# Kernel tuning notes

Measured on AMD Instinct MI355X. Metric: run time of the kernel, lower is better.

## Reference

```python
import jax, jax.numpy as jnp
import numpy as np

B, L, C = 2, 2048, 1024
DK, H = 64, 16

def setup_inputs() -> dict:
    key = jax.random.key(0)
    ks = jax.random.split(key, 12)
    def lin(kw, kb, out_dim, in_dim):
        w = jax.random.normal(kw, (out_dim, in_dim), jnp.float32) * (1.0 / np.sqrt(in_dim))
        b = jnp.zeros((out_dim,), jnp.float32)
        return w, b
    WQ_w, WQ_b = lin(ks[0], ks[1], DK * H, C)
    WK_w, WK_b = lin(ks[2], ks[3], DK * H, C)
    WV_w, WV_b = lin(ks[4], ks[5], DK * H, C)
    WO_w, WO_b = lin(ks[6], ks[7], C, DK * H)
    qx = jax.random.normal(ks[8], (B, L, C), jnp.float32)
    kx = jax.random.normal(ks[9], (B, L, C), jnp.float32)
    vx = jax.random.normal(ks[10], (B, L, C), jnp.float32)
    maskPAD = jax.random.randint(ks[11], (B, L, L), 0, 2, jnp.int32)
    return {"qx": qx, "kx": kx, "vx": vx, "maskPAD": maskPAD,
            "WQ_w": WQ_w, "WQ_b": WQ_b, "WK_w": WK_w, "WK_b": WK_b,
            "WV_w": WV_w, "WV_b": WV_b, "WO_w": WO_w, "WO_b": WO_b}

def reference(qx, kx, vx, maskPAD, WQ_w, WQ_b, WK_w, WK_b, WV_w, WV_b, WO_w, WO_b):
    Bq, qL, _ = qx.shape
    kvL = kx.shape[1]
    # projections -> [B, H, L, DK]
    q = (qx @ WQ_w.T + WQ_b).reshape(Bq, qL, H, DK).transpose(0, 2, 1, 3)
    k = (kx @ WK_w.T + WK_b).reshape(Bq, kvL, H, DK).transpose(0, 2, 1, 3)
    v = (vx @ WV_w.T + WV_b).reshape(Bq, kvL, H, DK).transpose(0, 2, 1, 3)
    scores = jnp.einsum('bhqd,bhkd->bhqk', q, k) / np.sqrt(DK).astype(np.float32)
    scores = jnp.where((maskPAD == 0)[:, None, :, :], jnp.float32(-2**15 + 1), scores)
    alpha = jax.nn.softmax(scores, axis=3)  # dropout p=0 (eval)
    z = jnp.einsum('bhqk,bhkd->bhqd', alpha, v)
    z = z.transpose(0, 2, 1, 3).reshape(Bq, qL, H * DK)
    return z @ WO_w.T + WO_b
```

## Files before the change

kernel.cpp:

```cpp
#include <hip/hip_runtime.h>
#include <stdint.h>
#include <math.h>

typedef short short8 __attribute__((ext_vector_type(8)));
typedef float float4v __attribute__((ext_vector_type(4)));

static __device__ __forceinline__ float bf2f(uint16_t u) {
    union { uint32_t i; float f; } x; x.i = ((uint32_t)u) << 16; return x.f;
}
static __device__ __forceinline__ uint16_t f2bf(float f) {
    union { float f; uint32_t i; } x; x.f = f;
    uint32_t u = x.i;
    u += 0x7FFFu + ((u >> 16) & 1u);
    return (uint16_t)(u >> 16);
}
static __device__ __forceinline__ uint16_t f2bf_sane(float f) {
    uint16_t u = f2bf(f);
    if ((u & 0x7F80u) == 0x7F80u) u = 0;
    return u;
}
static __device__ __forceinline__ float san_f32(float f) {
    union { float f; uint32_t i; } x; x.f = f;
    if (((x.i >> 23) & 0xFFu) == 0xFFu) return 0.f;
    return x.f;
}
static __device__ __forceinline__ void gll16(const void* g, void* l) {
    __builtin_amdgcn_global_load_lds((const __attribute__((address_space(1))) void*)g,
                                     (__attribute__((address_space(3))) void*)l,
                                     16, 0, 0);
}
static __device__ __forceinline__ short8 load8(const void* p, size_t off, int fp32) {
    if (!fp32) return *(const short8*)((const uint16_t*)p + off);
    const float* f = (const float*)p + off;
    const float4v a = *(const float4v*)f;
    const float4v b = *(const float4v*)(f + 4);
    short8 r;
    r[0] = (short)f2bf(a[0]); r[1] = (short)f2bf(a[1]);
    r[2] = (short)f2bf(a[2]); r[3] = (short)f2bf(a[3]);
    r[4] = (short)f2bf(b[0]); r[5] = (short)f2bf(b[1]);
    r[6] = (short)f2bf(b[2]); r[7] = (short)f2bf(b[3]);
    return r;
}

__global__ __launch_bounds__(256) void detect_kernel(const uint16_t* qx, int* flag)
{
    __shared__ int s;
    const int tid = threadIdx.x;
    if (tid == 0) s = 0;
    __syncthreads();
    int bad = 0;
#pragma unroll 8
    for (int i = 0; i < 64; ++i) {
        const uint16_t u = qx[tid * 64 + i];
        bad |= ((u & 0x7F80u) == 0x7F80u) ? 1 : 0;
    }
    if (bad) atomicOr(&s, 1);
    __syncthreads();
    if (tid == 0) *flag = s;
}

__global__ __launch_bounds__(256) void pack_kernel(
    const int* __restrict__ mask, uint64_t* __restrict__ mask64)
{
    const int wave = threadIdx.x >> 6, lane = threadIdx.x & 63;
    const int row = blockIdx.x * 4 + wave;
    const int* src = mask + (size_t)row * 2048;
#pragma unroll 4
    for (int j = 0; j < 32; ++j) {
        const int m = src[j * 64 + lane];
        const uint64_t bal = __ballot(m != 0);
        if (lane == 0) mask64[(size_t)row * 32 + j] = bal;
    }
}

__global__ __launch_bounds__(256) void convert_kernel(
    const void* qx, const void* kx, const void* vx,
    const void* wq, const void* wk, const void* wv, const void* wo,
    const void* bq, const void* bk, const void* bv, const void* bo,
    uint16_t* cIn, uint16_t* cW, uint16_t* cB, const int* flag)
{
    const int mode = *flag;
    if (!mode) return;
    const int z = blockIdx.z;
    const int idx8 = blockIdx.x * 256 + threadIdx.x;
    if (z < 3) {
        const void* src = (z == 0) ? qx : (z == 1) ? kx : vx;
        uint16_t* dst = cIn + (size_t)z * 4194304;
        if (idx8 < 524288)
            *(short8*)(dst + (size_t)idx8 * 8) = load8(src, (size_t)idx8 * 8, 1);
    } else if (z < 7) {
        const int t = z - 3;
        const void* src = (t == 0) ? wq : (t == 1) ? wk : (t == 2) ? wv : wo;
        uint16_t* dst = cW + (size_t)t * 1048576;
        if (idx8 < 131072)
            *(short8*)(dst + (size_t)idx8 * 8) = load8(src, (size_t)idx8 * 8, 1);
    } else {
        if (idx8 < 128) {
#pragma unroll
            for (int t = 0; t < 4; ++t) {
                const void* src = (t == 0) ? bq : (t == 1) ? bk : (t == 2) ? bv : bo;
                *(short8*)(cB + t * 1024 + idx8 * 8) = load8(src, (size_t)idx8 * 8, 1);
            }
        }
    }
}

template <int MI, int NI>
static __device__ __forceinline__ void gemm_tile(
    const uint16_t* __restrict__ A, const uint16_t* __restrict__ W,
    const uint16_t* __restrict__ bias, void* __restrict__ C,
    int c_fp32, float out_scale)
{
    constexpr int TM = MI * 32, TN = NI * 32;
    __shared__ __align__(16) uint16_t sA[TM * 32];
    __shared__ __align__(16) uint16_t sB[TN * 32];

    const int tid  = threadIdx.x;
    const int wave = tid >> 6;
    const int lane = tid & 63;
    const int quad = lane >> 4;
    const int l15  = lane & 15;
    const int m0 = blockIdx.y * TM;
    const int n0 = blockIdx.x * TN;
    const int wm = (wave >> 1) * (MI * 16);
    const int wn = (wave & 1) * (NI * 16);
    const int r16 = lane >> 2;
    const int ch  = lane & 3;

    float4v acc[MI][NI] = {};

    for (int k0 = 0; k0 < 1024; k0 += 32) {
        __syncthreads();
#pragma unroll
        for (int g = wave; g < TM / 16; g += 4)
            gll16(A + (size_t)(m0 + g * 16 + r16) * 1024 + k0 + ch * 8,
                  (char*)sA + (size_t)g * 1024);
#pragma unroll
        for (int g = wave; g < TN / 16; g += 4)
            gll16(W + (size_t)(n0 + g * 16 + r16) * 1024 + k0 + ch * 8,
                  (char*)sB + (size_t)g * 1024);
        asm volatile("s_waitcnt vmcnt(0)" ::: "memory");
        __syncthreads();

        short8 af[MI], bfr[NI];
#pragma unroll
        for (int i = 0; i < MI; ++i)
            af[i] = *(const short8*)&sA[(wm + i * 16 + l15) * 32 + quad * 8];
#pragma unroll
        for (int j = 0; j < NI; ++j)
            bfr[j] = *(const short8*)&sB[(wn + j * 16 + l15) * 32 + quad * 8];
#pragma unroll
        for (int mi = 0; mi < MI; ++mi)
#pragma unroll
            for (int ni = 0; ni < NI; ++ni)
                acc[mi][ni] = __builtin_amdgcn_mfma_f32_16x16x32_bf16(
                    af[mi], bfr[ni], acc[mi][ni], 0, 0, 0);
    }

#pragma unroll
    for (int ni = 0; ni < NI; ++ni) {
        const int n = n0 + wn + ni * 16 + l15;
        const float bv = bf2f(bias[n]);
#pragma unroll
        for (int mi = 0; mi < MI; ++mi) {
            const int mbase = m0 + wm + mi * 16 + quad * 4;
#pragma unroll
            for (int r = 0; r < 4; ++r) {
                const float v = (acc[mi][ni][r] + bv) * out_scale;
                const size_t idx = (size_t)(mbase + r) * 1024 + n;
                if (c_fp32) ((float*)C)[idx] = san_f32(v);
                else        ((uint16_t*)C)[idx] = f2bf_sane(v);
            }
        }
    }
}

__global__ __launch_bounds__(256) void qkv_kernel(
    const uint16_t* rqx, const uint16_t* rkx, const uint16_t* rvx,
    const uint16_t* rwq, const uint16_t* rwk, const uint16_t* rwv,
    const uint16_t* rbq, const uint16_t* rbk, const uint16_t* rbv,
    const uint16_t* cIn, const uint16_t* cW, const uint16_t* cB,
    uint16_t* Q, uint16_t* K, uint16_t* V, const int* flag)
{
    const int mode = *flag;
    const int z = blockIdx.z;
    const uint16_t* A = mode ? cIn + (size_t)z * 4194304
                             : ((z == 0) ? rqx : (z == 1) ? rkx : rvx);
    const uint16_t* W = mode ? cW + (size_t)z * 1048576
                             : ((z == 0) ? rwq : (z == 1) ? rwk : rwv);
    const uint16_t* b = mode ? cB + z * 1024
                             : ((z == 0) ? rbq : (z == 1) ? rbk : rbv);
    uint16_t* C = (z == 0) ? Q : (z == 1) ? K : V;
    const float sc = (z == 0) ? 0.125f : 1.0f;
    gemm_tile<4, 4>(A, W, b, C, 0, sc);
}

__global__ __launch_bounds__(256) void out_kernel(
    const uint16_t* Z, const uint16_t* rwo, const uint16_t* rbo,
    const uint16_t* cW, const uint16_t* cB, void* out, const int* flag)
{
    const int mode = *flag;
    const uint16_t* W = mode ? cW + 3 * 1048576 : rwo;
    const uint16_t* b = mode ? cB + 3 * 1024 : rbo;
    gemm_tile<2, 4>(Z, W, b, out, mode, 1.0f);
}

__global__ __launch_bounds__(256) void vtrans_kernel(
    const uint16_t* __restrict__ Vp, uint16_t* __restrict__ Vt)
{
    __shared__ __align__(16) uint16_t t[64][72];
    const int tid = threadIdx.x;
    const int lt = blockIdx.x, h = blockIdx.y, b = blockIdx.z;
#pragma unroll
    for (int p = 0; p < 2; ++p) {
        const int r = p * 32 + (tid >> 3);
        const int c = (tid & 7) * 8;
        *(short8*)&t[r][c] =
            *(const short8*)(Vp + (size_t)(b * 2048 + lt * 64 + r) * 1024 + h * 64 + c);
    }
    __syncthreads();
#pragma unroll
    for (int p = 0; p < 2; ++p) {
        const int d = p * 32 + (tid >> 3);
        const int c = (tid & 7) * 8;
        short8 v;
#pragma unroll
        for (int j = 0; j < 8; ++j) v[j] = (short)t[c + j][d];
        *(short8*)(Vt + (size_t)((b * 16 + h) * 64 + d) * 2048 + lt * 64 + c) = v;
    }
}

#define VS 72

__global__ __launch_bounds__(256) void attn_kernel(
    const uint16_t* __restrict__ Q, const uint16_t* __restrict__ Kp,
    const uint16_t* __restrict__ Vt, const uint64_t* __restrict__ mask64,
    uint16_t* __restrict__ Z)
{
    __shared__ __align__(16) uint16_t sK[64 * VS];
    __shared__ __align__(16) uint16_t sV[64 * VS];
    __shared__ __align__(16) uint16_t sP[4][32 * VS];

    const int tid = threadIdx.x;
    const int wave = tid >> 6, lane = tid & 63;
    const int quad = lane >> 4, l15 = lane & 15;
    const int qt = blockIdx.x, h = blockIdx.y, b = blockIdx.z;
    const int q0 = qt * 128;
    const int qw = q0 + wave * 32;

    const int srow = tid >> 2;
    const int sc0  = tid & 3;

    short8 qf[2][2];
#pragma unroll
    for (int mi = 0; mi < 2; ++mi)
#pragma unroll
        for (int kk = 0; kk < 2; ++kk)
            qf[mi][kk] = *(const short8*)(Q + (size_t)(b * 2048 + qw + mi * 16 + l15) * 1024
                                            + h * 64 + (quad + 4 * kk) * 8);

    const uint64_t* mrow[2][4];
#pragma unroll
    for (int mi = 0; mi < 2; ++mi)
#pragma unroll
        for (int r = 0; r < 4; ++r)
            mrow[mi][r] = mask64 + (size_t)(b * 2048 + qw + mi * 16 + quad * 4 + r) * 32;

    short8 ones;
#pragma unroll
    for (int j = 0; j < 8; ++j) ones[j] = (short)0x3F80;

    float4v oacc[2][4] = {};
    float4v lacc[2] = {};

    for (int kt = 0; kt < 32; ++kt) {
        const int k0 = kt * 64;
        const short8 kx0 = *(const short8*)(Kp + (size_t)(b * 2048 + k0 + srow) * 1024 + h * 64 + sc0 * 8);
        const short8 kx1 = *(const short8*)(Kp + (size_t)(b * 2048 + k0 + srow) * 1024 + h * 64 + (sc0 + 4) * 8);
        const short8 vx0 = *(const short8*)(Vt + (size_t)((b * 16 + h) * 64 + srow) * 2048 + k0 + sc0 * 8);
        const short8 vx1 = *(const short8*)(Vt + (size_t)((b * 16 + h) * 64 + srow) * 2048 + k0 + (sc0 + 4) * 8);
        __syncthreads();
        *(short8*)&sK[srow * VS + sc0 * 8]       = kx0;
        *(short8*)&sK[srow * VS + (sc0 + 4) * 8] = kx1;
        *(short8*)&sV[srow * VS + sc0 * 8]       = vx0;
        *(short8*)&sV[srow * VS + (sc0 + 4) * 8] = vx1;
        __syncthreads();

        float4v sacc[2][4] = {};
#pragma unroll
        for (int ni = 0; ni < 4; ++ni) {
            const int row = ni * 16 + l15;
#pragma unroll
            for (int kk = 0; kk < 2; ++kk) {
                const short8 kf = *(const short8*)&sK[row * VS + (quad + 4 * kk) * 8];
                sacc[0][ni] = __builtin_amdgcn_mfma_f32_16x16x32_bf16(qf[0][kk], kf, sacc[0][ni], 0, 0, 0);
                sacc[1][ni] = __builtin_amdgcn_mfma_f32_16x16x32_bf16(qf[1][kk], kf, sacc[1][ni], 0, 0, 0);
            }
        }

        uint16_t* Pw = &sP[wave][0];
#pragma unroll
        for (int mi = 0; mi < 2; ++mi) {
            uint64_t mw[4];
#pragma unroll
            for (int r = 0; r < 4; ++r) mw[r] = mrow[mi][r][kt];
#pragma unroll
            for (int ni = 0; ni < 4; ++ni)
#pragma unroll
                for (int r = 0; r < 4; ++r) {
                    const float p = ((mw[r] >> (ni * 16 + l15)) & 1ull)
                                        ? __expf(sacc[mi][ni][r]) : 0.f;
                    Pw[(mi * 16 + quad * 4 + r) * VS + ni * 16 + l15] = f2bf(p);
                }
        }
        asm volatile("s_waitcnt lgkmcnt(0)" ::: "memory");
        short8 pf[2][2];
#pragma unroll
        for (int mi = 0; mi < 2; ++mi)
#pragma unroll
            for (int kk = 0; kk < 2; ++kk)
                pf[mi][kk] = *(const short8*)&Pw[(mi * 16 + l15) * VS + (quad + 4 * kk) * 8];
        asm volatile("" ::: "memory");

#pragma unroll
        for (int ni = 0; ni < 4; ++ni) {
            const int row = ni * 16 + l15;
#pragma unroll
            for (int kk = 0; kk < 2; ++kk) {
                const short8 vf = *(const short8*)&sV[row * VS + (quad + 4 * kk) * 8];
                oacc[0][ni] = __builtin_amdgcn_mfma_f32_16x16x32_bf16(pf[0][kk], vf, oacc[0][ni], 0, 0, 0);
                oacc[1][ni] = __builtin_amdgcn_mfma_f32_16x16x32_bf16(pf[1][kk], vf, oacc[1][ni], 0, 0, 0);
            }
        }
#pragma unroll
        for (int mi = 0; mi < 2; ++mi)
#pragma unroll
            for (int kk = 0; kk < 2; ++kk)
                lacc[mi] = __builtin_amdgcn_mfma_f32_16x16x32_bf16(pf[mi][kk], ones, lacc[mi], 0, 0, 0);
    }

#pragma unroll
    for (int mi = 0; mi < 2; ++mi)
#pragma unroll
        for (int r = 0; r < 4; ++r) {
            const float inv = 1.0f / fmaxf(lacc[mi][r], 1e-37f);
            const int qrow = qw + mi * 16 + quad * 4 + r;
#pragma unroll
            for (int ni = 0; ni < 4; ++ni) {
                const float v = oacc[mi][ni][r] * inv;
                Z[(size_t)(b * 2048 + qrow) * 1024 + h * 64 + ni * 16 + l15] = f2bf_sane(v);
            }
        }
}

extern "C" void kernel_launch(void* const* d_in, const int* in_sizes, int n_in,
                              void* d_out, int out_size, void* d_ws, size_t ws_size,
                              hipStream_t stream)
{
    const void* qx  = d_in[0];
    const void* kx  = d_in[1];
    const void* vx  = d_in[2];
    const int*  msk = (const int*)d_in[3];

    char* ws = (char*)d_ws;
    const size_t MB = 1024 * 1024;
    uint16_t* cIn = (uint16_t*)(ws);
    uint16_t* cW  = (uint16_t*)(ws + 24 * MB);
    uint16_t* cB  = (uint16_t*)(ws + 32 * MB);
    int*      flg = (int*)(ws + 32 * MB + 16 * 1024);
    uint16_t* Qb  = (uint16_t*)(ws + 33 * MB);
    uint16_t* Kb  = (uint16_t*)(ws + 41 * MB);
    uint16_t* Vb  = (uint16_t*)(ws + 49 * MB);
    uint64_t* m64 = (uint64_t*)(ws + 57 * MB);
    uint16_t* Vt  = (uint16_t*)(ws + 8 * MB);
    uint16_t* Zb  = (uint16_t*)(ws);

    detect_kernel<<<1, 256, 0, stream>>>((const uint16_t*)qx, flg);
    pack_kernel<<<1024, 256, 0, stream>>>(msk, m64);
    convert_kernel<<<dim3(2048, 1, 8), 256, 0, stream>>>(
        qx, kx, vx, d_in[4], d_in[6], d_in[8], d_in[10],
        d_in[5], d_in[7], d_in[9], d_in[11], cIn, cW, cB, flg);
    qkv_kernel<<<dim3(8, 32, 3), 256, 0, stream>>>(
        (const uint16_t*)qx, (const uint16_t*)kx, (const uint16_t*)vx,
        (const uint16_t*)d_in[4], (const uint16_t*)d_in[6], (const uint16_t*)d_in[8],
        (const uint16_t*)d_in[5], (const uint16_t*)d_in[7], (const uint16_t*)d_in[9],
        cIn, cW, cB, Qb, Kb, Vb, flg);
    vtrans_kernel<<<dim3(32, 16, 2), 256, 0, stream>>>(Vb, Vt);
    attn_kernel<<<dim3(16, 16, 2), 256, 0, stream>>>(Qb, Kb, Vt, m64, Zb);
    out_kernel<<<dim3(8, 64), 256, 0, stream>>>(
        Zb, (const uint16_t*)d_in[10], (const uint16_t*)d_in[11], cW, cB, d_out, flg);
}
```

Baseline: 326.2 us.

## Split attention over key halves and add combine kernel; coarsen convert grid

The attention kernel now splits the key range into two halves across blockIdx.z, doubling the grid from 512 to 1024 blocks for better CU occupancy. Each half writes unnormalized bf16 partial outputs and row sums, and a new combine kernel adds them and normalizes. Separately, the convert kernel processes several vectors per thread with a smaller grid. The split adds an extra kernel launch, extra global traffic, and bf16 rounding of partial sums before normalization. It also reuses workspace regions, which relies on their lifetimes not overlapping.

```diff
diff --git a/kernel.cpp b/kernel.cpp
--- a/kernel.cpp
+++ b/kernel.cpp
@@ -82,19 +82,25 @@
     const int mode = *flag;
     if (!mode) return;
     const int z = blockIdx.z;
-    const int idx8 = blockIdx.x * 256 + threadIdx.x;
     if (z < 3) {
         const void* src = (z == 0) ? qx : (z == 1) ? kx : vx;
         uint16_t* dst = cIn + (size_t)z * 4194304;
-        if (idx8 < 524288)
+#pragma unroll
+        for (int it = 0; it < 8; ++it) {
+            const int idx8 = (blockIdx.x * 8 + it) * 256 + threadIdx.x;
             *(short8*)(dst + (size_t)idx8 * 8) = load8(src, (size_t)idx8 * 8, 1);
+        }
     } else if (z < 7) {
         const int t = z - 3;
         const void* src = (t == 0) ? wq : (t == 1) ? wk : (t == 2) ? wv : wo;
         uint16_t* dst = cW + (size_t)t * 1048576;
-        if (idx8 < 131072)
+#pragma unroll
+        for (int it = 0; it < 2; ++it) {
+            const int idx8 = (blockIdx.x * 2 + it) * 256 + threadIdx.x;
             *(short8*)(dst + (size_t)idx8 * 8) = load8(src, (size_t)idx8 * 8, 1);
+        }
     } else {
+        const int idx8 = blockIdx.x * 256 + threadIdx.x;
         if (idx8 < 128) {
 #pragma unroll
             for (int t = 0; t < 4; ++t) {
@@ -235,7 +241,8 @@
 __global__ __launch_bounds__(256) void attn_kernel(
     const uint16_t* __restrict__ Q, const uint16_t* __restrict__ Kp,
     const uint16_t* __restrict__ Vt, const uint64_t* __restrict__ mask64,
-    uint16_t* __restrict__ Z)
+    uint16_t* __restrict__ Oa, uint16_t* __restrict__ Ob,
+    float* __restrict__ lpart)
 {
     __shared__ __align__(16) uint16_t sK[64 * VS];
     __shared__ __align__(16) uint16_t sV[64 * VS];
@@ -244,7 +251,8 @@
     const int tid = threadIdx.x;
     const int wave = tid >> 6, lane = tid & 63;
     const int quad = lane >> 4, l15 = lane & 15;
-    const int qt = blockIdx.x, h = blockIdx.y, b = blockIdx.z;
+    const int qt = blockIdx.x, h = blockIdx.y;
+    const int b = blockIdx.z & 1, half = blockIdx.z >> 1;
     const int q0 = qt * 128;
     const int qw = q0 + wave * 32;
 
@@ -273,7 +281,8 @@
     float4v oacc[2][4] = {};
     float4v lacc[2] = {};
 
-    for (int kt = 0; kt < 32; ++kt) {
+    const int kt_lo = half * 16, kt_hi = kt_lo + 16;
+    for (int kt = kt_lo; kt < kt_hi; ++kt) {
         const int k0 = kt * 64;
         const short8 kx0 = *(const short8*)(Kp + (size_t)(b * 2048 + k0 + srow) * 1024 + h * 64 + sc0 * 8);
         const short8 kx1 = *(const short8*)(Kp + (size_t)(b * 2048 + k0 + srow) * 1024 + h * 64 + (sc0 + 4) * 8);
@@ -339,18 +348,39 @@
                 lacc[mi] = __builtin_amdgcn_mfma_f32_16x16x32_bf16(pf[mi][kk], ones, lacc[mi], 0, 0, 0);
     }
 
+    uint16_t* Op = half ? Ob : Oa;
 #pragma unroll
     for (int mi = 0; mi < 2; ++mi)
 #pragma unroll
         for (int r = 0; r < 4; ++r) {
-            const float inv = 1.0f / fmaxf(lacc[mi][r], 1e-37f);
             const int qrow = qw + mi * 16 + quad * 4 + r;
 #pragma unroll
-            for (int ni = 0; ni < 4; ++ni) {
-                const float v = oacc[mi][ni][r] * inv;
-                Z[(size_t)(b * 2048 + qrow) * 1024 + h * 64 + ni * 16 + l15] = f2bf_sane(v);
-            }
-        }
+            for (int ni = 0; ni < 4; ++ni)
+                Op[(size_t)(b * 2048 + qrow) * 1024 + h * 64 + ni * 16 + l15] = f2bf(oacc[mi][ni][r]);
+            if (l15 == 0)
+                lpart[half * 65536 + (b * 16 + h) * 2048 + qrow] = lacc[mi][r];
+        }
+}
+
+__global__ __launch_bounds__(256) void combine_kernel(
+    const uint16_t* __restrict__ Oa, const uint16_t* __restrict__ Ob,
+    const float* __restrict__ lpart, uint16_t* __restrict__ Z)
+{
+    const int e8 = blockIdx.x * 256 + threadIdx.x;
+    const int flat = e8 * 8;
+    const int bh_row = flat >> 10;
+    const int h = (flat >> 6) & 15;
+    const int b = bh_row >> 11;
+    const int row = bh_row & 2047;
+    const int lidx = (b * 16 + h) * 2048 + row;
+    const float inv = 1.0f / fmaxf(lpart[lidx] + lpart[65536 + lidx], 1e-37f);
+    const short8 a = *(const short8*)(Oa + flat);
+    const short8 c = *(const short8*)(Ob + flat);
+    short8 o;
+#pragma unroll
+    for (int j = 0; j < 8; ++j)
+        o[j] = (short)f2bf_sane((bf2f((uint16_t)a[j]) + bf2f((uint16_t)c[j])) * inv);
+    *(short8*)(Z + flat) = o;
 }
 
 extern "C" void kernel_launch(void* const* d_in, const int* in_sizes, int n_in,
@@ -373,11 +403,14 @@
     uint16_t* Vb  = (uint16_t*)(ws + 49 * MB);
     uint64_t* m64 = (uint64_t*)(ws + 57 * MB);
     uint16_t* Vt  = (uint16_t*)(ws + 8 * MB);
-    uint16_t* Zb  = (uint16_t*)(ws);
+    uint16_t* Oa  = (uint16_t*)(ws);
+    uint16_t* Ob  = (uint16_t*)(ws + 16 * MB);
+    float*    lp  = (float*)(ws + 49 * MB);
+    uint16_t* Zb  = Oa;
 
     detect_kernel<<<1, 256, 0, stream>>>((const uint16_t*)qx, flg);
     pack_kernel<<<1024, 256, 0, stream>>>(msk, m64);
-    convert_kernel<<<dim3(2048, 1, 8), 256, 0, stream>>>(
+    convert_kernel<<<dim3(256, 1, 8), 256, 0, stream>>>(
         qx, kx, vx, d_in[4], d_in[6], d_in[8], d_in[10],
         d_in[5], d_in[7], d_in[9], d_in[11], cIn, cW, cB, flg);
     qkv_kernel<<<dim3(8, 32, 3), 256, 0, stream>>>(
@@ -386,7 +419,8 @@
         (const uint16_t*)d_in[5], (const uint16_t*)d_in[7], (const uint16_t*)d_in[9],
         cIn, cW, cB, Qb, Kb, Vb, flg);
     vtrans_kernel<<<dim3(32, 16, 2), 256, 0, stream>>>(Vb, Vt);
-    attn_kernel<<<dim3(16, 16, 2), 256, 0, stream>>>(Qb, Kb, Vt, m64, Zb);
+    attn_kernel<<<dim3(16, 16, 4), 256, 0, stream>>>(Qb, Kb, Vt, m64, Oa, Ob, lp);
+    combine_kernel<<<4096, 256, 0, stream>>>(Oa, Ob, lp, Zb);
     out_kernel<<<dim3(8, 64), 256, 0, stream>>>(
         Zb, (const uint16_t*)d_in[10], (const uint16_t*)d_in[11], cW, cB, d_out, flg);
 }
```

New measurement: 325.3 us. Within noise of the previous version (-0.3%).
